# Optimization experiments

Measured on AMD Instinct MI355X. Metric: run time of the kernel, lower is better.

Reference implementation:

```python
import jax, jax.numpy as jnp
import numpy as np

V = 50257      # vocab_size
EMB = 300      # emb_size
H = 512        # mcan_flat_out_size (GRU hidden)
HS = 256       # hidden_size (object proposal feature dim)
BH = 256       # bi_hidden_size (encoder output feature dim)
NP = 256       # num_proposal
ML = 50        # max_length (lang seq len)
AL = 20        # answer length -> 19 decode steps
NEG = -1e9


def setup_inputs() -> dict:
    key = jax.random.key(0)
    ks = jax.random.split(key, 30)
    s = 0.02
    n = lambda k, sh: (s * jax.random.normal(k, sh)).astype(jnp.float32)
    d = {}
    d["input_tok"] = jax.random.randint(ks[0], (1,), 0, V, dtype=jnp.int32)
    d["hidden"] = jax.random.normal(ks[1], (1, 1, H), jnp.float32)
    d["encoder_outputs"] = jax.random.normal(ks[2], (ML, BH), jnp.float32)
    d["object_proposals"] = jax.random.normal(ks[3], (NP, HS), jnp.float32)
    d["object_mask"] = jax.random.randint(ks[4], (1, NP), 0, 2, dtype=jnp.int32)
    d["lang_mask"] = jax.random.randint(ks[5], (1, ML), 0, 2, dtype=jnp.int32)
    d["answer_to_vocab"] = jax.random.randint(ks[6], (AL,), 0, V, dtype=jnp.int32)
    # learned params (dropout treated as eval/identity)
    d["emb"] = n(ks[7], (V, EMB))
    cin = H + EMB  # 812
    d["attn_w1"] = n(ks[8], (256, cin)); d["attn_b1"] = jnp.zeros((256,), jnp.float32)
    d["attn_w2"] = n(ks[9], (ML, 256)); d["attn_b2"] = jnp.zeros((ML,), jnp.float32)
    d["attn_op_w1"] = n(ks[10], (256, cin)); d["attn_op_b1"] = jnp.zeros((256,), jnp.float32)
    d["attn_op_w2"] = n(ks[11], (NP, 256)); d["attn_op_b2"] = jnp.zeros((NP,), jnp.float32)
    comb_in = HS + BH + EMB  # 812
    d["cmb_w1"] = n(ks[12], (512, comb_in)); d["cmb_b1"] = jnp.zeros((512,), jnp.float32)
    d["cmb_w2"] = n(ks[13], (H, 512)); d["cmb_b2"] = jnp.zeros((H,), jnp.float32)
    d["gru_w_ih"] = n(ks[14], (3 * H, H)); d["gru_w_hh"] = n(ks[15], (3 * H, H))
    d["gru_b_ih"] = jnp.zeros((3 * H,), jnp.float32); d["gru_b_hh"] = jnp.zeros((3 * H,), jnp.float32)
    d["out_w"] = n(ks[16], (V, H)); d["out_b"] = jnp.zeros((V,), jnp.float32)
    return d


def reference(input_tok, hidden, encoder_outputs, object_proposals, object_mask,
              lang_mask, answer_to_vocab, emb, attn_w1, attn_b1, attn_w2, attn_b2,
              attn_op_w1, attn_op_b1, attn_op_w2, attn_op_b2, cmb_w1, cmb_b1,
              cmb_w2, cmb_b2, gru_w_ih, gru_w_hh, gru_b_ih, gru_b_hh, out_w, out_b):
    obj_m = object_mask.astype(bool)   # [1, NP]
    lang_m = lang_mask.astype(bool)    # [1, ML]
    # teacher forcing: step i embeds answer_to_vocab[i] (step 0 uses input_tok)
    tokens = jnp.concatenate([input_tok, answer_to_vocab[1:-1]])  # [AL-1]

    def step(h, tok):
        # h: [1,1,H]
        x = jax.nn.relu(emb[tok])[None, :]                     # [1,EMB]
        cat = jnp.concatenate([x, h[0]], axis=1)               # [1, EMB+H]
        # object attention
        a_op = jax.nn.relu(cat @ attn_op_w1.T + attn_op_b1) @ attn_op_w2.T + attn_op_b2
        a_op = jax.nn.softmax(jnp.where(obj_m, NEG, a_op), axis=1)   # [1,NP]
        ctx_op = a_op @ object_proposals                       # [1,HS]
        # language attention
        a_l = jax.nn.relu(cat @ attn_w1.T + attn_b1) @ attn_w2.T + attn_b2
        a_l = jax.nn.softmax(jnp.where(lang_m, NEG, a_l), axis=1)    # [1,ML]
        ctx = a_l @ encoder_outputs                            # [1,BH]
        comb = jnp.concatenate([x, ctx, ctx_op], axis=1)       # [1, EMB+BH+HS]
        g = jax.nn.relu(jax.nn.relu(comb @ cmb_w1.T + cmb_b1) @ cmb_w2.T + cmb_b2)  # [1,H]
        # GRU cell (torch gate order: r, z, n)
        gi = g @ gru_w_ih.T + gru_b_ih
        gh = h[0] @ gru_w_hh.T + gru_b_hh
        i_r, i_z, i_n = jnp.split(gi, 3, axis=1)
        h_r, h_z, h_n = jnp.split(gh, 3, axis=1)
        r = jax.nn.sigmoid(i_r + h_r)
        z = jax.nn.sigmoid(i_z + h_z)
        nn_ = jnp.tanh(i_n + r * h_n)
        h_new = (1.0 - z) * nn_ + z * h[0]                     # [1,H]
        logits = h_new @ out_w.T + out_b                       # [1,V]
        return h_new[None], (logits, a_l, a_op)

    _, (logits, attn_w, attn_ob_w) = jax.lax.scan(step, hidden, tokens)
    # logits: [AL-1,1,V]; attn_w: [AL-1,1,ML]; attn_ob_w: [AL-1,1,NP]
    return logits, attn_w, attn_ob_w
```

## Files before the change

kernel.cpp:

```cpp
#include <hip/hip_runtime.h>
#include <math.h>

#define T_STEPS 19
#define V 50257
#define EMB 300
#define HDIM 512
#define NP 256
#define ML 50
#define CIN 812
#define NEGV -1e9f
#define NBLK 64

#define OFF_X      0
#define OFF_POP    5700
#define OFF_PL     10564
#define OFF_PC     15428
#define OFF_HS     25156
#define OFF_H1OP   35396
#define OFF_H1L    35652
#define OFF_C1     37444
#define OFF_G      37956
#define OFF_LOGOP  38468
#define OFF_LOGL   38724
#define OFF_MPROP  38788
#define OFF_MENC   169860
#define OFF_BAR    195460

#define OUT_LOGITS 0
#define OUT_ATTW   ((long)T_STEPS * V)
#define OUT_ATTOB  (OUT_ATTW + (long)T_STEPS * ML)

__device__ __forceinline__ float wred(float v) {
  v += __shfl_xor(v, 32, 64);
  v += __shfl_xor(v, 16, 64);
  v += __shfl_xor(v, 8, 64);
  v += __shfl_xor(v, 4, 64);
  v += __shfl_xor(v, 2, 64);
  v += __shfl_xor(v, 1, 64);
  return v;
}

__device__ __forceinline__ float dot4(float4 a, float4 b) {
  return a.x * b.x + a.y * b.y + a.z * b.z + a.w * b.w;
}

__device__ __forceinline__ void gstore(float* p, float v) {
  __hip_atomic_store(p, v, __ATOMIC_RELAXED, __HIP_MEMORY_SCOPE_AGENT);
}
__device__ __forceinline__ float ld1c(const float* p) {
  return __hip_atomic_load(p, __ATOMIC_RELAXED, __HIP_MEMORY_SCOPE_AGENT);
}
__device__ __forceinline__ float2 ld2c(const float* p) {
  unsigned long long u = __hip_atomic_load((const unsigned long long*)p,
                                           __ATOMIC_RELAXED, __HIP_MEMORY_SCOPE_AGENT);
  float2 r;
  r.x = __uint_as_float((unsigned)u);
  r.y = __uint_as_float((unsigned)(u >> 32));
  return r;
}
__device__ __forceinline__ float4 ld4c(const float* p) {
  float2 a = ld2c(p), b = ld2c(p + 2);
  return make_float4(a.x, a.y, b.x, b.y);
}

__device__ __forceinline__ void gbar(float* wsb, unsigned bar) {
  asm volatile("s_waitcnt vmcnt(0)" ::: "memory");
  __syncthreads();
  unsigned* flags = (unsigned*)(wsb + OFF_BAR) + 16;
  if (threadIdx.x == 0) {
    __hip_atomic_store(flags + 16 * blockIdx.x, bar, __ATOMIC_RELAXED, __HIP_MEMORY_SCOPE_AGENT);
  }
  asm volatile("" ::: "memory");
  if (threadIdx.x < 64) {
    unsigned* f = flags + 16 * threadIdx.x;
    while (__hip_atomic_load(f, __ATOMIC_RELAXED, __HIP_MEMORY_SCOPE_AGENT) < bar) {
      __builtin_amdgcn_s_sleep(1);
    }
  }
  __syncthreads();
}

__global__ void k_pre1(const int* __restrict__ tok0, const int* __restrict__ ans,
                       const float* __restrict__ emb, const float* __restrict__ hidden,
                       float* __restrict__ ws) {
  int tid = blockIdx.x * 256 + threadIdx.x;
  if (tid < T_STEPS * EMB) {
    int s = tid / EMB, j = tid - s * EMB;
    int t = (s == 0) ? tok0[0] : ans[s];
    float v = emb[(long)t * EMB + j];
    ws[OFF_X + tid] = v > 0.f ? v : 0.f;
  } else {
    int k = tid - T_STEPS * EMB;
    if (k < HDIM) ws[OFF_HS + k] = hidden[k];
  }
}

__global__ void k_pre2(const float* __restrict__ w1op, const float* __restrict__ b1op,
                       const float* __restrict__ w1l,  const float* __restrict__ b1l,
                       const float* __restrict__ wc1,  const float* __restrict__ bc1,
                       float* __restrict__ ws) {
  int gw = (blockIdx.x * 256 + threadIdx.x) >> 6;
  int lane = threadIdx.x & 63;
  int s = gw >> 10;
  int rr = gw & 1023;
  if (s >= T_STEPS) return;
  const float* wrow; const float* bias; float* dst; int r;
  if (rr < 256)      { r = rr;       wrow = w1op + (long)r * CIN; bias = b1op; dst = ws + OFF_POP + s * 256 + r; }
  else if (rr < 512) { r = rr - 256; wrow = w1l  + (long)r * CIN; bias = b1l;  dst = ws + OFF_PL  + s * 256 + r; }
  else               { r = rr - 512; wrow = wc1  + (long)r * CIN; bias = bc1;  dst = ws + OFF_PC  + s * 512 + r; }
  const float* x = ws + OFF_X + s * EMB;
  float acc = 0.f;
#pragma unroll
  for (int it = 0; it < 5; ++it) {
    int j = it * 64 + lane;
    if (j < EMB) acc += wrow[j] * x[j];
  }
  acc = wred(acc);
  if (lane == 0) *dst = acc + bias[r];
}

#define LDSF 12850
__global__ void __launch_bounds__(256) k_mprep(const float* __restrict__ cw1,
                                               const float* __restrict__ prop,
                                               const float* __restrict__ enc,
                                               float* __restrict__ ws) {
  __shared__ float lds[LDSF];
  int tid = threadIdx.x, r = blockIdx.x;
  float acc = 0.f;
  for (int kc = 0; kc < 8; ++kc) {
    __syncthreads();
#pragma unroll
    for (int i = 0; i < 8; ++i) {
      int f = tid + 256 * i; int row = f >> 3, q = f & 7;
      float4 v = *(const float4*)(prop + (long)row * 256 + kc * 32 + 4 * q);
      float* p = lds + row * 33 + 4 * q;
      p[0] = v.x; p[1] = v.y; p[2] = v.z; p[3] = v.w;
    }
    __syncthreads();
    const float* wbase = cw1 + (long)r * CIN + 556 + kc * 32;
    const float* pl = lds + tid * 33;
#pragma unroll
    for (int k4 = 0; k4 < 8; ++k4) {
      float4 w4 = *(const float4*)(wbase + 4 * k4);
      const float* pp = pl + 4 * k4;
      acc += w4.x * pp[0] + w4.y * pp[1] + w4.z * pp[2] + w4.w * pp[3];
    }
  }
  ws[OFF_MPROP + (long)r * 256 + tid] = acc;
  __syncthreads();
  for (int i = 0; i < 13; ++i) {
    int f = tid + 256 * i;
    if (f < 3200) {
      int row = f >> 6, q = f & 63;
      float4 v = *(const float4*)(enc + (long)row * 256 + 4 * q);
      float* p = lds + row * 257 + 4 * q;
      p[0] = v.x; p[1] = v.y; p[2] = v.z; p[3] = v.w;
    }
  }
  __syncthreads();
  if (tid < ML) {
    const float* wb2 = cw1 + (long)r * CIN + 300;
    const float* el = lds + tid * 257;
    float a2 = 0.f;
#pragma unroll 8
    for (int k = 0; k < 256; ++k) a2 += wb2[k] * el[k];
    ws[OFF_MENC + (long)r * ML + tid] = a2;
  }
}

__global__ void __launch_bounds__(256) k_recur(
    const float* __restrict__ w1op, const float* __restrict__ w1l,
    const float* __restrict__ whh,  const float* __restrict__ bhh,
    const float* __restrict__ w2op, const float* __restrict__ b2op,
    const float* __restrict__ w2l,  const float* __restrict__ b2l,
    const int* __restrict__ obj_mask, const int* __restrict__ lang_mask,
    const float* __restrict__ wc2,  const float* __restrict__ bc2,
    const float* __restrict__ wih,  const float* __restrict__ bih,
    float* ws, float* __restrict__ out) {
  const int tid = threadIdx.x;
  const int lane = tid & 63;
  const int wv = (blockIdx.x << 2) + (tid >> 6);
  const int r0 = 2 * wv, r1 = 2 * wv + 1;
  unsigned bar = 1;
  __shared__ float red[256];
  __shared__ __align__(16) float sm_aop[256];
  __shared__ float sm_al[64];

  for (int s = 0; s < T_STEPS; ++s) {
    float ghr0, ghz0, ghn0, ghr1, ghz1, ghn1;
    {
      const float* h = ws + OFF_HS + s * HDIM;
      float4 ha = ld4c(h + 4 * lane);
      float4 hb = ld4c(h + 256 + 4 * lane);
      const float* wa0 = (r0 < 256) ? (w1op + (long)r0 * CIN + 300) : (w1l + (long)(r0 - 256) * CIN + 300);
      const float* wa1 = (r1 < 256) ? (w1op + (long)r1 * CIN + 300) : (w1l + (long)(r1 - 256) * CIN + 300);
      float a0 = dot4(*(const float4*)(wa0 + 4 * lane), ha) + dot4(*(const float4*)(wa0 + 256 + 4 * lane), hb);
      float a1 = dot4(*(const float4*)(wa1 + 4 * lane), ha) + dot4(*(const float4*)(wa1 + 256 + 4 * lane), hb);
      const float* p0 = whh + (long)r0 * HDIM;
      const float* p1 = whh + (long)(r0 + 512) * HDIM;
      const float* p2 = whh + (long)(r0 + 1024) * HDIM;
      const float* p3 = whh + (long)r1 * HDIM;
      const float* p4 = whh + (long)(r1 + 512) * HDIM;
      const float* p5 = whh + (long)(r1 + 1024) * HDIM;
      float b0 = dot4(*(const float4*)(p0 + 4 * lane), ha) + dot4(*(const float4*)(p0 + 256 + 4 * lane), hb);
      float b1 = dot4(*(const float4*)(p1 + 4 * lane), ha) + dot4(*(const float4*)(p1 + 256 + 4 * lane), hb);
      float b2 = dot4(*(const float4*)(p2 + 4 * lane), ha) + dot4(*(const float4*)(p2 + 256 + 4 * lane), hb);
      float b3 = dot4(*(const float4*)(p3 + 4 * lane), ha) + dot4(*(const float4*)(p3 + 256 + 4 * lane), hb);
      float b4 = dot4(*(const float4*)(p4 + 4 * lane), ha) + dot4(*(const float4*)(p4 + 256 + 4 * lane), hb);
      float b5 = dot4(*(const float4*)(p5 + 4 * lane), ha) + dot4(*(const float4*)(p5 + 256 + 4 * lane), hb);
      a0 = wred(a0); a1 = wred(a1);
      b0 = wred(b0); b1 = wred(b1); b2 = wred(b2);
      b3 = wred(b3); b4 = wred(b4); b5 = wred(b5);
      ghr0 = b0 + bhh[r0]; ghz0 = b1 + bhh[512 + r0]; ghn0 = b2 + bhh[1024 + r0];
      ghr1 = b3 + bhh[r1]; ghz1 = b4 + bhh[512 + r1]; ghn1 = b5 + bhh[1024 + r1];
      if (lane == 0) {
        float v0 = a0 + ((r0 < 256) ? ws[OFF_POP + s * 256 + r0] : ws[OFF_PL + s * 256 + (r0 - 256)]);
        float v1 = a1 + ((r1 < 256) ? ws[OFF_POP + s * 256 + r1] : ws[OFF_PL + s * 256 + (r1 - 256)]);
        float* d0 = (r0 < 256) ? (ws + OFF_H1OP + r0) : (ws + OFF_H1L + (r0 - 256));
        float* d1 = (r1 < 256) ? (ws + OFF_H1OP + r1) : (ws + OFF_H1L + (r1 - 256));
        gstore(d0, v0 > 0.f ? v0 : 0.f);
        gstore(d1, v1 > 0.f ? v1 : 0.f);
      }
    }
    gbar(ws, bar++);
    {
      float4 h1 = ld4c(ws + OFF_H1OP + 4 * lane);
      const float* wr = w2op + (long)wv * 256;
      float acc = wred(dot4(*(const float4*)(wr + 4 * lane), h1));
      if (lane == 0) gstore(ws + OFF_LOGOP + wv, acc + b2op[wv]);
      if (wv < ML) {
        float4 h1l = ld4c(ws + OFF_H1L + 4 * lane);
        const float* wrl = w2l + (long)wv * 256;
        float accl = wred(dot4(*(const float4*)(wrl + 4 * lane), h1l));
        if (lane == 0) gstore(ws + OFF_LOGL + wv, accl + b2l[wv]);
      }
    }
    gbar(ws, bar++);
    {
      float lv = ld1c(ws + OFF_LOGOP + tid);
      float vo = (obj_mask[tid] != 0) ? NEGV : lv;
      red[tid] = vo; __syncthreads();
      for (int st = 128; st > 0; st >>= 1) { if (tid < st) red[tid] = fmaxf(red[tid], red[tid + st]); __syncthreads(); }
      float mo = red[0]; __syncthreads();
      float eo = expf(vo - mo);
      red[tid] = eo; __syncthreads();
      for (int st = 128; st > 0; st >>= 1) { if (tid < st) red[tid] += red[tid + st]; __syncthreads(); }
      float aop = eo / red[0];
      sm_aop[tid] = aop;
      __syncthreads();
      float ll = (tid < ML) ? ld1c(ws + OFF_LOGL + tid) : 0.f;
      float vl = (tid < ML) ? ((lang_mask[tid] != 0) ? NEGV : ll) : -3e38f;
      red[tid] = vl; __syncthreads();
      for (int st = 128; st > 0; st >>= 1) { if (tid < st) red[tid] = fmaxf(red[tid], red[tid + st]); __syncthreads(); }
      float ml_ = red[0]; __syncthreads();
      float el = (tid < ML) ? expf(vl - ml_) : 0.f;
      red[tid] = el; __syncthreads();
      for (int st = 128; st > 0; st >>= 1) { if (tid < st) red[tid] += red[tid + st]; __syncthreads(); }
      float al = el / red[0];
      if (tid < 64) sm_al[tid] = (tid < ML) ? al : 0.f;
      __syncthreads();
      if (blockIdx.x == 0) {
        out[OUT_ATTOB + (long)s * NP + tid] = aop;
        if (tid < ML) out[OUT_ATTW + (long)s * ML + tid] = al;
      }
      float4 a4 = *(const float4*)(&sm_aop[4 * lane]);
      const float* mp0 = ws + OFF_MPROP + (long)r0 * 256;
      const float* mp1 = ws + OFF_MPROP + (long)r1 * 256;
      float acc0 = dot4(*(const float4*)(mp0 + 4 * lane), a4);
      float acc1 = dot4(*(const float4*)(mp1 + 4 * lane), a4);
      if (lane < ML) {
        float alv = sm_al[lane];
        acc0 += ws[OFF_MENC + (long)r0 * ML + lane] * alv;
        acc1 += ws[OFF_MENC + (long)r1 * ML + lane] * alv;
      }
      acc0 = wred(acc0); acc1 = wred(acc1);
      if (lane == 0) {
        float v0 = acc0 + ws[OFF_PC + s * HDIM + r0];
        float v1 = acc1 + ws[OFF_PC + s * HDIM + r1];
        gstore(ws + OFF_C1 + r0, v0 > 0.f ? v0 : 0.f);
        gstore(ws + OFF_C1 + r1, v1 > 0.f ? v1 : 0.f);
      }
    }
    gbar(ws, bar++);
    {
      float4 ca = ld4c(ws + OFF_C1 + 4 * lane);
      float4 cb = ld4c(ws + OFF_C1 + 256 + 4 * lane);
      const float* q0 = wc2 + (long)r0 * HDIM;
      const float* q1 = wc2 + (long)r1 * HDIM;
      float acc0 = dot4(*(const float4*)(q0 + 4 * lane), ca) + dot4(*(const float4*)(q0 + 256 + 4 * lane), cb);
      float acc1 = dot4(*(const float4*)(q1 + 4 * lane), ca) + dot4(*(const float4*)(q1 + 256 + 4 * lane), cb);
      acc0 = wred(acc0); acc1 = wred(acc1);
      if (lane == 0) {
        float v0 = acc0 + bc2[r0];
        float v1 = acc1 + bc2[r1];
        gstore(ws + OFF_G + r0, v0 > 0.f ? v0 : 0.f);
        gstore(ws + OFF_G + r1, v1 > 0.f ? v1 : 0.f);
      }
    }
    gbar(ws, bar++);
    {
      float4 ga = ld4c(ws + OFF_G + 4 * lane);
      float4 gb = ld4c(ws + OFF_G + 256 + 4 * lane);
      const float* p0 = wih + (long)r0 * HDIM;
      const float* p1 = wih + (long)(r0 + 512) * HDIM;
      const float* p2 = wih + (long)(r0 + 1024) * HDIM;
      const float* p3 = wih + (long)r1 * HDIM;
      const float* p4 = wih + (long)(r1 + 512) * HDIM;
      const float* p5 = wih + (long)(r1 + 1024) * HDIM;
      float a0 = dot4(*(const float4*)(p0 + 4 * lane), ga) + dot4(*(const float4*)(p0 + 256 + 4 * lane), gb);
      float a1 = dot4(*(const float4*)(p1 + 4 * lane), ga) + dot4(*(const float4*)(p1 + 256 + 4 * lane), gb);
      float a2 = dot4(*(const float4*)(p2 + 4 * lane), ga) + dot4(*(const float4*)(p2 + 256 + 4 * lane), gb);
      float a3 = dot4(*(const float4*)(p3 + 4 * lane), ga) + dot4(*(const float4*)(p3 + 256 + 4 * lane), gb);
      float a4_ = dot4(*(const float4*)(p4 + 4 * lane), ga) + dot4(*(const float4*)(p4 + 256 + 4 * lane), gb);
      float a5 = dot4(*(const float4*)(p5 + 4 * lane), ga) + dot4(*(const float4*)(p5 + 256 + 4 * lane), gb);
      a0 = wred(a0); a1 = wred(a1); a2 = wred(a2);
      a3 = wred(a3); a4_ = wred(a4_); a5 = wred(a5);
      if (lane == 0) {
        float ir0 = a0 + bih[r0], iz0 = a1 + bih[512 + r0], in0 = a2 + bih[1024 + r0];
        float rg0 = 1.f / (1.f + expf(-(ir0 + ghr0)));
        float zg0 = 1.f / (1.f + expf(-(iz0 + ghz0)));
        float ng0 = tanhf(in0 + rg0 * ghn0);
        float hp0 = ld1c(ws + OFF_HS + s * HDIM + r0);
        gstore(ws + OFF_HS + (s + 1) * HDIM + r0, (1.f - zg0) * ng0 + zg0 * hp0);
        float ir1 = a3 + bih[r1], iz1 = a4_ + bih[512 + r1], in1 = a5 + bih[1024 + r1];
        float rg1 = 1.f / (1.f + expf(-(ir1 + ghr1)));
        float zg1 = 1.f / (1.f + expf(-(iz1 + ghz1)));
        float ng1 = tanhf(in1 + rg1 * ghn1);
        float hp1 = ld1c(ws + OFF_HS + s * HDIM + r1);
        gstore(ws + OFF_HS + (s + 1) * HDIM + r1, (1.f - zg1) * ng1 + zg1 * hp1);
      }
    }
    gbar(ws, bar++);
  }
}

__global__ void __launch_bounds__(256) k_final2(const float* __restrict__ ow,
                                                const float* __restrict__ ob,
                                                const float* __restrict__ ws,
                                                float* __restrict__ out) {
  __shared__ __align__(16) float wl[256 * 36];
  __shared__ __align__(16) float hl[T_STEPS * 512];
  int tid = threadIdx.x;
  long rbase = (long)blockIdx.x * 256;
  for (int i = tid; i < T_STEPS * 512; i += 256) hl[i] = ws[OFF_HS + 512 + i];
  float4 st[8];
#pragma unroll
  for (int i = 0; i < 8; ++i) {
    int f = tid + 256 * i; int row = f >> 3, q = f & 7;
    long r = rbase + row;
    st[i] = (r < V) ? *(const float4*)(ow + r * 512 + 4 * q) : make_float4(0.f, 0.f, 0.f, 0.f);
  }
  float acc[T_STEPS];
#pragma unroll
  for (int s = 0; s < T_STEPS; ++s) acc[s] = 0.f;
  __syncthreads();
  for (int c = 0; c < 16; ++c) {
#pragma unroll
    for (int i = 0; i < 8; ++i) {
      int f = tid + 256 * i; int row = f >> 3, q = f & 7;
      float* p = wl + row * 36 + 4 * q;
      p[0] = st[i].x; p[1] = st[i].y; p[2] = st[i].z; p[3] = st[i].w;
    }
    __syncthreads();
    if (c < 15) {
#pragma unroll
      for (int i = 0; i < 8; ++i) {
        int f = tid + 256 * i; int row = f >> 3, q = f & 7;
        long r = rbase + row;
        st[i] = (r < V) ? *(const float4*)(ow + r * 512 + (c + 1) * 32 + 4 * q) : make_float4(0.f, 0.f, 0.f, 0.f);
      }
    }
    const float* wp = wl + tid * 36;
#pragma unroll
    for (int kq = 0; kq < 8; ++kq) {
      float4 w4 = *(const float4*)(wp + 4 * kq);
      const float* hb = hl + c * 32 + 4 * kq;
#pragma unroll
      for (int s = 0; s < T_STEPS; ++s) {
        float4 h4 = *(const float4*)(hb + s * 512);
        acc[s] += dot4(w4, h4);
      }
    }
    __syncthreads();
  }
  long r = rbase + tid;
  if (r < V) {
    float b = ob[r];
#pragma unroll
    for (int s = 0; s < T_STEPS; ++s) out[OUT_LOGITS + (long)s * V + r] = acc[s] + b;
  }
}

extern "C" void kernel_launch(void* const* d_in, const int* in_sizes, int n_in,
                              void* d_out, int out_size, void* d_ws, size_t ws_size,
                              hipStream_t stream) {
  const int*   input_tok  = (const int*)d_in[0];
  const float* hidden     = (const float*)d_in[1];
  const float* enc        = (const float*)d_in[2];
  const float* prop       = (const float*)d_in[3];
  const int*   obj_mask   = (const int*)d_in[4];
  const int*   lang_mask  = (const int*)d_in[5];
  const int*   ans        = (const int*)d_in[6];
  const float* emb        = (const float*)d_in[7];
  const float* attn_w1    = (const float*)d_in[8];
  const float* attn_b1    = (const float*)d_in[9];
  const float* attn_w2    = (const float*)d_in[10];
  const float* attn_b2    = (const float*)d_in[11];
  const float* attn_op_w1 = (const float*)d_in[12];
  const float* attn_op_b1 = (const float*)d_in[13];
  const float* attn_op_w2 = (const float*)d_in[14];
  const float* attn_op_b2 = (const float*)d_in[15];
  const float* cmb_w1     = (const float*)d_in[16];
  const float* cmb_b1     = (const float*)d_in[17];
  const float* cmb_w2     = (const float*)d_in[18];
  const float* cmb_b2     = (const float*)d_in[19];
  const float* gw_ih      = (const float*)d_in[20];
  const float* gw_hh      = (const float*)d_in[21];
  const float* gb_ih      = (const float*)d_in[22];
  const float* gb_hh      = (const float*)d_in[23];
  const float* out_w      = (const float*)d_in[24];
  const float* out_b      = (const float*)d_in[25];
  float* out = (float*)d_out;
  float* ws  = (float*)d_ws;

  hipMemsetAsync((char*)d_ws + (size_t)OFF_BAR * 4, 0, 8448, stream);
  k_pre1<<<25, 256, 0, stream>>>(input_tok, ans, emb, hidden, ws);
  k_pre2<<<4864, 256, 0, stream>>>(attn_op_w1, attn_op_b1, attn_w1, attn_b1, cmb_w1, cmb_b1, ws);
  k_mprep<<<512, 256, 0, stream>>>(cmb_w1, prop, enc, ws);
  k_recur<<<NBLK, 256, 0, stream>>>(attn_op_w1, attn_w1, gw_hh, gb_hh,
                                    attn_op_w2, attn_op_b2, attn_w2, attn_b2,
                                    obj_mask, lang_mask, cmb_w2, cmb_b2,
                                    gw_ih, gb_ih, ws, out);
  k_final2<<<(V + 255) / 256, 256, 0, stream>>>(out_w, out_b, ws, out);
}
```

Baseline: 419.2 us.

## Split grid barriers into arrive/wait, drop one barrier, prefetch weights across waits

```diff
diff --git a/kernel.cpp b/kernel.cpp
--- a/kernel.cpp
+++ b/kernel.cpp
@@ -20,11 +20,11 @@
 #define OFF_H1L    35652
 #define OFF_C1     37444
 #define OFF_G      37956
-#define OFF_LOGOP  38468
-#define OFF_LOGL   38724
 #define OFF_MPROP  38788
 #define OFF_MENC   169860
-#define OFF_BAR    195460
+#define OFF_W2OPT  195460
+#define OFF_W2LT   260996
+#define OFF_BAR    277380
 
 #define OUT_LOGITS 0
 #define OUT_ATTW   ((long)T_STEPS * V)
@@ -63,16 +63,17 @@
   return make_float4(a.x, a.y, b.x, b.y);
 }
 
-__device__ __forceinline__ void gbar(float* wsb, unsigned bar) {
+__device__ __forceinline__ void gbar_arrive(float* wsb, unsigned bar) {
   asm volatile("s_waitcnt vmcnt(0)" ::: "memory");
   __syncthreads();
-  unsigned* flags = (unsigned*)(wsb + OFF_BAR) + 16;
   if (threadIdx.x == 0) {
+    unsigned* flags = (unsigned*)(wsb + OFF_BAR) + 16;
     __hip_atomic_store(flags + 16 * blockIdx.x, bar, __ATOMIC_RELAXED, __HIP_MEMORY_SCOPE_AGENT);
   }
-  asm volatile("" ::: "memory");
+}
+__device__ __forceinline__ void gbar_wait(float* wsb, unsigned bar) {
   if (threadIdx.x < 64) {
-    unsigned* f = flags + 16 * threadIdx.x;
+    unsigned* f = (unsigned*)(wsb + OFF_BAR) + 16 + 16 * threadIdx.x;
     while (__hip_atomic_load(f, __ATOMIC_RELAXED, __HIP_MEMORY_SCOPE_AGENT) < bar) {
       __builtin_amdgcn_s_sleep(1);
     }
@@ -168,11 +169,18 @@
   }
 }
 
+__global__ void k_pre4(const float* __restrict__ w2op, const float* __restrict__ w2l,
+                       float* __restrict__ ws) {
+  int r = blockIdx.x;
+  int k = threadIdx.x;
+  ws[OFF_W2OPT + (k >> 2) * 1024 + r * 4 + (k & 3)] = w2op[(long)r * 256 + k];
+  if (r < ML) ws[OFF_W2LT + (k >> 2) * 256 + r * 4 + (k & 3)] = w2l[(long)r * 256 + k];
+}
+
 __global__ void __launch_bounds__(256) k_recur(
     const float* __restrict__ w1op, const float* __restrict__ w1l,
     const float* __restrict__ whh,  const float* __restrict__ bhh,
-    const float* __restrict__ w2op, const float* __restrict__ b2op,
-    const float* __restrict__ w2l,  const float* __restrict__ b2l,
+    const float* __restrict__ b2op, const float* __restrict__ b2l,
     const int* __restrict__ obj_mask, const int* __restrict__ lang_mask,
     const float* __restrict__ wc2,  const float* __restrict__ bc2,
     const float* __restrict__ wih,  const float* __restrict__ bih,
@@ -185,6 +193,8 @@
   __shared__ float red[256];
   __shared__ __align__(16) float sm_aop[256];
   __shared__ float sm_al[64];
+  __shared__ __align__(16) float sm_h1op[256];
+  __shared__ __align__(16) float sm_h1l[256];
 
   for (int s = 0; s < T_STEPS; ++s) {
     float ghr0, ghz0, ghn0, ghr1, ghz1, ghn1;
@@ -196,6 +206,16 @@
       const float* wa1 = (r1 < 256) ? (w1op + (long)r1 * CIN + 300) : (w1l + (long)(r1 - 256) * CIN + 300);
       float a0 = dot4(*(const float4*)(wa0 + 4 * lane), ha) + dot4(*(const float4*)(wa0 + 256 + 4 * lane), hb);
       float a1 = dot4(*(const float4*)(wa1 + 4 * lane), ha) + dot4(*(const float4*)(wa1 + 256 + 4 * lane), hb);
+      a0 = wred(a0); a1 = wred(a1);
+      if (lane == 0) {
+        float v0 = a0 + ((r0 < 256) ? ws[OFF_POP + s * 256 + r0] : ws[OFF_PL + s * 256 + (r0 - 256)]);
+        float v1 = a1 + ((r1 < 256) ? ws[OFF_POP + s * 256 + r1] : ws[OFF_PL + s * 256 + (r1 - 256)]);
+        float* d0 = (r0 < 256) ? (ws + OFF_H1OP + r0) : (ws + OFF_H1L + (r0 - 256));
+        float* d1 = (r1 < 256) ? (ws + OFF_H1OP + r1) : (ws + OFF_H1L + (r1 - 256));
+        gstore(d0, v0 > 0.f ? v0 : 0.f);
+        gstore(d1, v1 > 0.f ? v1 : 0.f);
+      }
+      gbar_arrive(ws, bar);
       const float* p0 = whh + (long)r0 * HDIM;
       const float* p1 = whh + (long)(r0 + 512) * HDIM;
       const float* p2 = whh + (long)(r0 + 1024) * HDIM;
@@ -208,37 +228,37 @@
       float b3 = dot4(*(const float4*)(p3 + 4 * lane), ha) + dot4(*(const float4*)(p3 + 256 + 4 * lane), hb);
       float b4 = dot4(*(const float4*)(p4 + 4 * lane), ha) + dot4(*(const float4*)(p4 + 256 + 4 * lane), hb);
       float b5 = dot4(*(const float4*)(p5 + 4 * lane), ha) + dot4(*(const float4*)(p5 + 256 + 4 * lane), hb);
-      a0 = wred(a0); a1 = wred(a1);
       b0 = wred(b0); b1 = wred(b1); b2 = wred(b2);
       b3 = wred(b3); b4 = wred(b4); b5 = wred(b5);
       ghr0 = b0 + bhh[r0]; ghz0 = b1 + bhh[512 + r0]; ghn0 = b2 + bhh[1024 + r0];
       ghr1 = b3 + bhh[r1]; ghz1 = b4 + bhh[512 + r1]; ghn1 = b5 + bhh[1024 + r1];
-      if (lane == 0) {
-        float v0 = a0 + ((r0 < 256) ? ws[OFF_POP + s * 256 + r0] : ws[OFF_PL + s * 256 + (r0 - 256)]);
-        float v1 = a1 + ((r1 < 256) ? ws[OFF_POP + s * 256 + r1] : ws[OFF_PL + s * 256 + (r1 - 256)]);
-        float* d0 = (r0 < 256) ? (ws + OFF_H1OP + r0) : (ws + OFF_H1L + (r0 - 256));
-        float* d1 = (r1 < 256) ? (ws + OFF_H1OP + r1) : (ws + OFF_H1L + (r1 - 256));
-        gstore(d0, v0 > 0.f ? v0 : 0.f);
-        gstore(d1, v1 > 0.f ? v1 : 0.f);
-      }
-    }
-    gbar(ws, bar++);
+      gbar_wait(ws, bar); bar++;
+    }
+    float4 wc0a, wc0b, wc1a, wc1b;
     {
-      float4 h1 = ld4c(ws + OFF_H1OP + 4 * lane);
-      const float* wr = w2op + (long)wv * 256;
-      float acc = wred(dot4(*(const float4*)(wr + 4 * lane), h1));
-      if (lane == 0) gstore(ws + OFF_LOGOP + wv, acc + b2op[wv]);
-      if (wv < ML) {
-        float4 h1l = ld4c(ws + OFF_H1L + 4 * lane);
-        const float* wrl = w2l + (long)wv * 256;
-        float accl = wred(dot4(*(const float4*)(wrl + 4 * lane), h1l));
-        if (lane == 0) gstore(ws + OFF_LOGL + wv, accl + b2l[wv]);
-      }
-    }
-    gbar(ws, bar++);
-    {
-      float lv = ld1c(ws + OFF_LOGOP + tid);
-      float vo = (obj_mask[tid] != 0) ? NEGV : lv;
+      sm_h1op[tid] = ld1c(ws + OFF_H1OP + tid);
+      sm_h1l[tid]  = ld1c(ws + OFF_H1L + tid);
+      __syncthreads();
+      float lo = b2op[tid];
+      const float* w2T = ws + OFF_W2OPT;
+#pragma unroll 8
+      for (int k4 = 0; k4 < 64; ++k4) {
+        float4 h4 = *(const float4*)(&sm_h1op[4 * k4]);
+        float4 w4 = *(const float4*)(&w2T[k4 * 1024 + tid * 4]);
+        lo += dot4(w4, h4);
+      }
+      float llg = 0.f;
+      if (tid < ML) {
+        llg = b2l[tid];
+        const float* wlT = ws + OFF_W2LT;
+#pragma unroll 8
+        for (int k4 = 0; k4 < 64; ++k4) {
+          float4 h4 = *(const float4*)(&sm_h1l[4 * k4]);
+          float4 w4 = *(const float4*)(&wlT[k4 * 256 + tid * 4]);
+          llg += dot4(w4, h4);
+        }
+      }
+      float vo = (obj_mask[tid] != 0) ? NEGV : lo;
       red[tid] = vo; __syncthreads();
       for (int st = 128; st > 0; st >>= 1) { if (tid < st) red[tid] = fmaxf(red[tid], red[tid + st]); __syncthreads(); }
       float mo = red[0]; __syncthreads();
@@ -248,8 +268,7 @@
       float aop = eo / red[0];
       sm_aop[tid] = aop;
       __syncthreads();
-      float ll = (tid < ML) ? ld1c(ws + OFF_LOGL + tid) : 0.f;
-      float vl = (tid < ML) ? ((lang_mask[tid] != 0) ? NEGV : ll) : -3e38f;
+      float vl = (tid < ML) ? ((lang_mask[tid] != 0) ? NEGV : llg) : -3e38f;
       red[tid] = vl; __syncthreads();
       for (int st = 128; st > 0; st >>= 1) { if (tid < st) red[tid] = fmaxf(red[tid], red[tid + st]); __syncthreads(); }
       float ml_ = red[0]; __syncthreads();
@@ -280,15 +299,21 @@
         gstore(ws + OFF_C1 + r0, v0 > 0.f ? v0 : 0.f);
         gstore(ws + OFF_C1 + r1, v1 > 0.f ? v1 : 0.f);
       }
-    }
-    gbar(ws, bar++);
+      gbar_arrive(ws, bar);
+      const float* q0 = wc2 + (long)r0 * HDIM;
+      const float* q1 = wc2 + (long)r1 * HDIM;
+      wc0a = *(const float4*)(q0 + 4 * lane);
+      wc0b = *(const float4*)(q0 + 256 + 4 * lane);
+      wc1a = *(const float4*)(q1 + 4 * lane);
+      wc1b = *(const float4*)(q1 + 256 + 4 * lane);
+      gbar_wait(ws, bar); bar++;
+    }
+    float4 wi0a, wi0b, wi1a, wi1b, wi2a, wi2b, wi3a, wi3b, wi4a, wi4b, wi5a, wi5b;
     {
       float4 ca = ld4c(ws + OFF_C1 + 4 * lane);
       float4 cb = ld4c(ws + OFF_C1 + 256 + 4 * lane);
-      const float* q0 = wc2 + (long)r0 * HDIM;
-      const float* q1 = wc2 + (long)r1 * HDIM;
-      float acc0 = dot4(*(const float4*)(q0 + 4 * lane), ca) + dot4(*(const float4*)(q0 + 256 + 4 * lane), cb);
-      float acc1 = dot4(*(const float4*)(q1 + 4 * lane), ca) + dot4(*(const float4*)(q1 + 256 + 4 * lane), cb);
+      float acc0 = dot4(wc0a, ca) + dot4(wc0b, cb);
+      float acc1 = dot4(wc1a, ca) + dot4(wc1b, cb);
       acc0 = wred(acc0); acc1 = wred(acc1);
       if (lane == 0) {
         float v0 = acc0 + bc2[r0];
@@ -296,23 +321,30 @@
         gstore(ws + OFF_G + r0, v0 > 0.f ? v0 : 0.f);
         gstore(ws + OFF_G + r1, v1 > 0.f ? v1 : 0.f);
       }
-    }
-    gbar(ws, bar++);
-    {
-      float4 ga = ld4c(ws + OFF_G + 4 * lane);
-      float4 gb = ld4c(ws + OFF_G + 256 + 4 * lane);
+      gbar_arrive(ws, bar);
       const float* p0 = wih + (long)r0 * HDIM;
       const float* p1 = wih + (long)(r0 + 512) * HDIM;
       const float* p2 = wih + (long)(r0 + 1024) * HDIM;
       const float* p3 = wih + (long)r1 * HDIM;
       const float* p4 = wih + (long)(r1 + 512) * HDIM;
       const float* p5 = wih + (long)(r1 + 1024) * HDIM;
-      float a0 = dot4(*(const float4*)(p0 + 4 * lane), ga) + dot4(*(const float4*)(p0 + 256 + 4 * lane), gb);
-      float a1 = dot4(*(const float4*)(p1 + 4 * lane), ga) + dot4(*(const float4*)(p1 + 256 + 4 * lane), gb);
-      float a2 = dot4(*(const float4*)(p2 + 4 * lane), ga) + dot4(*(const float4*)(p2 + 256 + 4 * lane), gb);
-      float a3 = dot4(*(const float4*)(p3 + 4 * lane), ga) + dot4(*(const float4*)(p3 + 256 + 4 * lane), gb);
-      float a4_ = dot4(*(const float4*)(p4 + 4 * lane), ga) + dot4(*(const float4*)(p4 + 256 + 4 * lane), gb);
-      float a5 = dot4(*(const float4*)(p5 + 4 * lane), ga) + dot4(*(const float4*)(p5 + 256 + 4 * lane), gb);
+      wi0a = *(const float4*)(p0 + 4 * lane); wi0b = *(const float4*)(p0 + 256 + 4 * lane);
+      wi1a = *(const float4*)(p1 + 4 * lane); wi1b = *(const float4*)(p1 + 256 + 4 * lane);
+      wi2a = *(const float4*)(p2 + 4 * lane); wi2b = *(const float4*)(p2 + 256 + 4 * lane);
+      wi3a = *(const float4*)(p3 + 4 * lane); wi3b = *(const float4*)(p3 + 256 + 4 * lane);
+      wi4a = *(const float4*)(p4 + 4 * lane); wi4b = *(const float4*)(p4 + 256 + 4 * lane);
+      wi5a = *(const float4*)(p5 + 4 * lane); wi5b = *(const float4*)(p5 + 256 + 4 * lane);
+      gbar_wait(ws, bar); bar++;
+    }
+    {
+      float4 ga = ld4c(ws + OFF_G + 4 * lane);
+      float4 gb = ld4c(ws + OFF_G + 256 + 4 * lane);
+      float a0 = dot4(wi0a, ga) + dot4(wi0b, gb);
+      float a1 = dot4(wi1a, ga) + dot4(wi1b, gb);
+      float a2 = dot4(wi2a, ga) + dot4(wi2b, gb);
+      float a3 = dot4(wi3a, ga) + dot4(wi3b, gb);
+      float a4_ = dot4(wi4a, ga) + dot4(wi4b, gb);
+      float a5 = dot4(wi5a, ga) + dot4(wi5b, gb);
       a0 = wred(a0); a1 = wred(a1); a2 = wred(a2);
       a3 = wred(a3); a4_ = wred(a4_); a5 = wred(a5);
       if (lane == 0) {
@@ -329,16 +361,18 @@
         float hp1 = ld1c(ws + OFF_HS + s * HDIM + r1);
         gstore(ws + OFF_HS + (s + 1) * HDIM + r1, (1.f - zg1) * ng1 + zg1 * hp1);
       }
-    }
-    gbar(ws, bar++);
-  }
-}
-
+      gbar_arrive(ws, bar);
+      gbar_wait(ws, bar); bar++;
+    }
+  }
+}
+
+#define WL(row, q) ((q) * 1032 + 4 * (row))
 __global__ void __launch_bounds__(256) k_final2(const float* __restrict__ ow,
                                                 const float* __restrict__ ob,
                                                 const float* __restrict__ ws,
                                                 float* __restrict__ out) {
-  __shared__ __align__(16) float wl[256 * 36];
+  __shared__ __align__(16) float wl[8 * 1032];
   __shared__ __align__(16) float hl[T_STEPS * 512];
   int tid = threadIdx.x;
   long rbase = (long)blockIdx.x * 256;
@@ -358,8 +392,7 @@
 #pragma unroll
     for (int i = 0; i < 8; ++i) {
       int f = tid + 256 * i; int row = f >> 3, q = f & 7;
-      float* p = wl + row * 36 + 4 * q;
-      p[0] = st[i].x; p[1] = st[i].y; p[2] = st[i].z; p[3] = st[i].w;
+      *(float4*)(&wl[WL(row, q)]) = st[i];
     }
     __syncthreads();
     if (c < 15) {
@@ -370,10 +403,9 @@
         st[i] = (r < V) ? *(const float4*)(ow + r * 512 + (c + 1) * 32 + 4 * q) : make_float4(0.f, 0.f, 0.f, 0.f);
       }
     }
-    const float* wp = wl + tid * 36;
 #pragma unroll
     for (int kq = 0; kq < 8; ++kq) {
-      float4 w4 = *(const float4*)(wp + 4 * kq);
+      float4 w4 = *(const float4*)(&wl[WL(tid, kq)]);
       const float* hb = hl + c * 32 + 4 * kq;
 #pragma unroll
       for (int s = 0; s < T_STEPS; ++s) {
@@ -427,8 +459,9 @@
   k_pre1<<<25, 256, 0, stream>>>(input_tok, ans, emb, hidden, ws);
   k_pre2<<<4864, 256, 0, stream>>>(attn_op_w1, attn_op_b1, attn_w1, attn_b1, cmb_w1, cmb_b1, ws);
   k_mprep<<<512, 256, 0, stream>>>(cmb_w1, prop, enc, ws);
+  k_pre4<<<256, 256, 0, stream>>>(attn_op_w2, attn_w2, ws);
   k_recur<<<NBLK, 256, 0, stream>>>(attn_op_w1, attn_w1, gw_hh, gb_hh,
-                                    attn_op_w2, attn_op_b2, attn_w2, attn_b2,
+                                    attn_op_b2, attn_b2,
                                     obj_mask, lang_mask, cmb_w2, cmb_b2,
                                     gw_ih, gb_ih, ws, out);
   k_final2<<<(V + 255) / 256, 256, 0, stream>>>(out_w, out_b, ws, out);
```

New measurement: 672.0 us. 1.6x slower.

## Replace grid barriers with NaN-poisoned per-step dataflow polling

Applied to the files above, without the earlier changes.

```diff
diff --git a/kernel.cpp b/kernel.cpp
--- a/kernel.cpp
+++ b/kernel.cpp
@@ -15,16 +15,24 @@
 #define OFF_POP    5700
 #define OFF_PL     10564
 #define OFF_PC     15428
-#define OFF_HS     25156
-#define OFF_H1OP   35396
-#define OFF_H1L    35652
-#define OFF_C1     37444
-#define OFF_G      37956
-#define OFF_LOGOP  38468
-#define OFF_LOGL   38724
-#define OFF_MPROP  38788
-#define OFF_MENC   169860
-#define OFF_BAR    195460
+#define OFF_MPROP  25156
+#define OFF_MENC   156228
+#define OFF_HS     181828
+#define OFF_H1OP   192068
+#define OFF_H1L    196932
+#define OFF_LOGOP  201796
+#define OFF_LOGL   206660
+#define OFF_C1     207876
+#define OFF_G      217604
+#define POISON_END 227332
+#define POISON_BYTES ((POISON_END - OFF_HS) * 4)
+
+#define H1OP_S(s) (OFF_H1OP + (s) * 256)
+#define H1L_S(s)  (OFF_H1L  + (s) * 256)
+#define LOGOP_S(s)(OFF_LOGOP+ (s) * 256)
+#define LOGL_S(s) (OFF_LOGL + (s) * 64)
+#define C1_S(s)   (OFF_C1   + (s) * 512)
+#define G_S(s)    (OFF_G    + (s) * 512)
 
 #define OUT_LOGITS 0
 #define OUT_ATTW   ((long)T_STEPS * V)
@@ -63,21 +71,18 @@
   return make_float4(a.x, a.y, b.x, b.y);
 }
 
-__device__ __forceinline__ void gbar(float* wsb, unsigned bar) {
-  asm volatile("s_waitcnt vmcnt(0)" ::: "memory");
-  __syncthreads();
-  unsigned* flags = (unsigned*)(wsb + OFF_BAR) + 16;
-  if (threadIdx.x == 0) {
-    __hip_atomic_store(flags + 16 * blockIdx.x, bar, __ATOMIC_RELAXED, __HIP_MEMORY_SCOPE_AGENT);
-  }
-  asm volatile("" ::: "memory");
-  if (threadIdx.x < 64) {
-    unsigned* f = flags + 16 * threadIdx.x;
-    while (__hip_atomic_load(f, __ATOMIC_RELAXED, __HIP_MEMORY_SCOPE_AGENT) < bar) {
-      __builtin_amdgcn_s_sleep(1);
-    }
-  }
-  __syncthreads();
+__device__ __forceinline__ int nan4(float4 v) {
+  return (v.x != v.x) | (v.y != v.y) | (v.z != v.z) | (v.w != v.w);
+}
+__device__ __forceinline__ float4 poll4(const float* p) {
+  float4 v = ld4c(p);
+  while (__any(nan4(v))) { __builtin_amdgcn_s_sleep(1); v = ld4c(p); }
+  return v;
+}
+__device__ __forceinline__ float poll1(const float* p) {
+  float v = ld1c(p);
+  while (__any(v != v)) { __builtin_amdgcn_s_sleep(1); v = ld1c(p); }
+  return v;
 }
 
 __global__ void k_pre1(const int* __restrict__ tok0, const int* __restrict__ ans,
@@ -181,7 +186,6 @@
   const int lane = tid & 63;
   const int wv = (blockIdx.x << 2) + (tid >> 6);
   const int r0 = 2 * wv, r1 = 2 * wv + 1;
-  unsigned bar = 1;
   __shared__ float red[256];
   __shared__ __align__(16) float sm_aop[256];
   __shared__ float sm_al[64];
@@ -190,8 +194,8 @@
     float ghr0, ghz0, ghn0, ghr1, ghz1, ghn1;
     {
       const float* h = ws + OFF_HS + s * HDIM;
-      float4 ha = ld4c(h + 4 * lane);
-      float4 hb = ld4c(h + 256 + 4 * lane);
+      float4 ha = poll4(h + 4 * lane);
+      float4 hb = poll4(h + 256 + 4 * lane);
       const float* wa0 = (r0 < 256) ? (w1op + (long)r0 * CIN + 300) : (w1l + (long)(r0 - 256) * CIN + 300);
       const float* wa1 = (r1 < 256) ? (w1op + (long)r1 * CIN + 300) : (w1l + (long)(r1 - 256) * CIN + 300);
       float a0 = dot4(*(const float4*)(wa0 + 4 * lane), ha) + dot4(*(const float4*)(wa0 + 256 + 4 * lane), hb);
@@ -216,28 +220,26 @@
       if (lane == 0) {
         float v0 = a0 + ((r0 < 256) ? ws[OFF_POP + s * 256 + r0] : ws[OFF_PL + s * 256 + (r0 - 256)]);
         float v1 = a1 + ((r1 < 256) ? ws[OFF_POP + s * 256 + r1] : ws[OFF_PL + s * 256 + (r1 - 256)]);
-        float* d0 = (r0 < 256) ? (ws + OFF_H1OP + r0) : (ws + OFF_H1L + (r0 - 256));
-        float* d1 = (r1 < 256) ? (ws + OFF_H1OP + r1) : (ws + OFF_H1L + (r1 - 256));
+        float* d0 = (r0 < 256) ? (ws + H1OP_S(s) + r0) : (ws + H1L_S(s) + (r0 - 256));
+        float* d1 = (r1 < 256) ? (ws + H1OP_S(s) + r1) : (ws + H1L_S(s) + (r1 - 256));
         gstore(d0, v0 > 0.f ? v0 : 0.f);
         gstore(d1, v1 > 0.f ? v1 : 0.f);
       }
     }
-    gbar(ws, bar++);
     {
-      float4 h1 = ld4c(ws + OFF_H1OP + 4 * lane);
+      float4 h1 = poll4(ws + H1OP_S(s) + 4 * lane);
       const float* wr = w2op + (long)wv * 256;
       float acc = wred(dot4(*(const float4*)(wr + 4 * lane), h1));
-      if (lane == 0) gstore(ws + OFF_LOGOP + wv, acc + b2op[wv]);
+      if (lane == 0) gstore(ws + LOGOP_S(s) + wv, acc + b2op[wv]);
       if (wv < ML) {
-        float4 h1l = ld4c(ws + OFF_H1L + 4 * lane);
+        float4 h1l = poll4(ws + H1L_S(s) + 4 * lane);
         const float* wrl = w2l + (long)wv * 256;
         float accl = wred(dot4(*(const float4*)(wrl + 4 * lane), h1l));
-        if (lane == 0) gstore(ws + OFF_LOGL + wv, accl + b2l[wv]);
-      }
-    }
-    gbar(ws, bar++);
+        if (lane == 0) gstore(ws + LOGL_S(s) + wv, accl + b2l[wv]);
+      }
+    }
     {
-      float lv = ld1c(ws + OFF_LOGOP + tid);
+      float lv = poll1(ws + LOGOP_S(s) + tid);
       float vo = (obj_mask[tid] != 0) ? NEGV : lv;
       red[tid] = vo; __syncthreads();
       for (int st = 128; st > 0; st >>= 1) { if (tid < st) red[tid] = fmaxf(red[tid], red[tid + st]); __syncthreads(); }
@@ -248,7 +250,8 @@
       float aop = eo / red[0];
       sm_aop[tid] = aop;
       __syncthreads();
-      float ll = (tid < ML) ? ld1c(ws + OFF_LOGL + tid) : 0.f;
+      float ll = 0.f;
+      if (tid < ML) ll = poll1(ws + LOGL_S(s) + tid);
       float vl = (tid < ML) ? ((lang_mask[tid] != 0) ? NEGV : ll) : -3e38f;
       red[tid] = vl; __syncthreads();
       for (int st = 128; st > 0; st >>= 1) { if (tid < st) red[tid] = fmaxf(red[tid], red[tid + st]); __syncthreads(); }
@@ -277,14 +280,13 @@
       if (lane == 0) {
         float v0 = acc0 + ws[OFF_PC + s * HDIM + r0];
         float v1 = acc1 + ws[OFF_PC + s * HDIM + r1];
-        gstore(ws + OFF_C1 + r0, v0 > 0.f ? v0 : 0.f);
-        gstore(ws + OFF_C1 + r1, v1 > 0.f ? v1 : 0.f);
-      }
-    }
-    gbar(ws, bar++);
+        gstore(ws + C1_S(s) + r0, v0 > 0.f ? v0 : 0.f);
+        gstore(ws + C1_S(s) + r1, v1 > 0.f ? v1 : 0.f);
+      }
+    }
     {
-      float4 ca = ld4c(ws + OFF_C1 + 4 * lane);
-      float4 cb = ld4c(ws + OFF_C1 + 256 + 4 * lane);
+      float4 ca = poll4(ws + C1_S(s) + 4 * lane);
+      float4 cb = poll4(ws + C1_S(s) + 256 + 4 * lane);
       const float* q0 = wc2 + (long)r0 * HDIM;
       const float* q1 = wc2 + (long)r1 * HDIM;
       float acc0 = dot4(*(const float4*)(q0 + 4 * lane), ca) + dot4(*(const float4*)(q0 + 256 + 4 * lane), cb);
@@ -293,14 +295,13 @@
       if (lane == 0) {
         float v0 = acc0 + bc2[r0];
         float v1 = acc1 + bc2[r1];
-        gstore(ws + OFF_G + r0, v0 > 0.f ? v0 : 0.f);
-        gstore(ws + OFF_G + r1, v1 > 0.f ? v1 : 0.f);
-      }
-    }
-    gbar(ws, bar++);
+        gstore(ws + G_S(s) + r0, v0 > 0.f ? v0 : 0.f);
+        gstore(ws + G_S(s) + r1, v1 > 0.f ? v1 : 0.f);
+      }
+    }
     {
-      float4 ga = ld4c(ws + OFF_G + 4 * lane);
-      float4 gb = ld4c(ws + OFF_G + 256 + 4 * lane);
+      float4 ga = poll4(ws + G_S(s) + 4 * lane);
+      float4 gb = poll4(ws + G_S(s) + 256 + 4 * lane);
       const float* p0 = wih + (long)r0 * HDIM;
       const float* p1 = wih + (long)(r0 + 512) * HDIM;
       const float* p2 = wih + (long)(r0 + 1024) * HDIM;
@@ -330,15 +331,15 @@
         gstore(ws + OFF_HS + (s + 1) * HDIM + r1, (1.f - zg1) * ng1 + zg1 * hp1);
       }
     }
-    gbar(ws, bar++);
-  }
-}
-
+  }
+}
+
+#define WL(row, q) ((q) * 1032 + 4 * (row))
 __global__ void __launch_bounds__(256) k_final2(const float* __restrict__ ow,
                                                 const float* __restrict__ ob,
                                                 const float* __restrict__ ws,
                                                 float* __restrict__ out) {
-  __shared__ __align__(16) float wl[256 * 36];
+  __shared__ __align__(16) float wl[8 * 1032];
   __shared__ __align__(16) float hl[T_STEPS * 512];
   int tid = threadIdx.x;
   long rbase = (long)blockIdx.x * 256;
@@ -358,8 +359,7 @@
 #pragma unroll
     for (int i = 0; i < 8; ++i) {
       int f = tid + 256 * i; int row = f >> 3, q = f & 7;
-      float* p = wl + row * 36 + 4 * q;
-      p[0] = st[i].x; p[1] = st[i].y; p[2] = st[i].z; p[3] = st[i].w;
+      *(float4*)(&wl[WL(row, q)]) = st[i];
     }
     __syncthreads();
     if (c < 15) {
@@ -370,10 +370,9 @@
         st[i] = (r < V) ? *(const float4*)(ow + r * 512 + (c + 1) * 32 + 4 * q) : make_float4(0.f, 0.f, 0.f, 0.f);
       }
     }
-    const float* wp = wl + tid * 36;
 #pragma unroll
     for (int kq = 0; kq < 8; ++kq) {
-      float4 w4 = *(const float4*)(wp + 4 * kq);
+      float4 w4 = *(const float4*)(&wl[WL(tid, kq)]);
       const float* hb = hl + c * 32 + 4 * kq;
 #pragma unroll
       for (int s = 0; s < T_STEPS; ++s) {
@@ -423,7 +422,7 @@
   float* out = (float*)d_out;
   float* ws  = (float*)d_ws;
 
-  hipMemsetAsync((char*)d_ws + (size_t)OFF_BAR * 4, 0, 8448, stream);
+  hipMemsetAsync((char*)d_ws + (size_t)OFF_HS * 4, 0xFF, POISON_BYTES, stream);
   k_pre1<<<25, 256, 0, stream>>>(input_tok, ans, emb, hidden, ws);
   k_pre2<<<4864, 256, 0, stream>>>(attn_op_w1, attn_op_b1, attn_w1, attn_b1, cmb_w1, cmb_b1, ws);
   k_mprep<<<512, 256, 0, stream>>>(cmb_w1, prop, enc, ws);
```

After: 573.6 us. +36.8%, slower.
